# Optimization experiments

Hardware: AMD Instinct MI355X
Metric: run time of the kernel (lower is better)

## Reference

```python
import jax, jax.numpy as jnp
import numpy as np

WS = (8, 8)          # window size
NUM_HEADS = 16
C = 512
B_ = 2048            # batch * num_windows
NW = 256             # num_windows per image (mask dim)
N = WS[0] * WS[1]    # tokens per window = 64


def _relative_position_index():
    coords = np.stack(np.meshgrid(np.arange(WS[0]), np.arange(WS[1]), indexing='ij'))  # [2,Wh,Ww]
    flat = coords.reshape(2, -1)                         # [2,N]
    rel = flat[:, :, None] - flat[:, None, :]            # [2,N,N]
    rel = rel.transpose(1, 2, 0).astype(np.int32)        # [N,N,2]
    rel[..., 0] += WS[0] - 1
    rel[..., 1] += WS[1] - 1
    rel[..., 0] *= 2 * WS[1] - 1
    return jnp.asarray(rel.sum(-1))                      # [N,N] in [0, 225)


def setup_inputs() -> dict:
    key = jax.random.key(0)
    ks = jax.random.split(key, 8)
    return {
        'x': jax.random.normal(ks[0], (B_, N, C), jnp.float32),
        'mask': jax.random.normal(ks[1], (NW, N, N), jnp.float32),
        'qkv_w': jax.random.normal(ks[2], (3 * C, C), jnp.float32) * 0.02,
        'q_bias': jax.random.normal(ks[3], (C,), jnp.float32) * 0.02,
        'v_bias': jax.random.normal(ks[4], (C,), jnp.float32) * 0.02,
        'rpb_table': jax.random.normal(ks[5], ((2 * WS[0] - 1) * (2 * WS[1] - 1), NUM_HEADS), jnp.float32) * 0.02,
        'proj_w': jax.random.normal(ks[6], (C, C), jnp.float32) * 0.02,
        'proj_b': jax.random.normal(ks[7], (C,), jnp.float32) * 0.02,
        'rel_index': _relative_position_index(),
    }


def reference(x, mask, qkv_w, q_bias, v_bias, rpb_table, proj_w, proj_b, rel_index):
    Bw, n, c = x.shape
    h = NUM_HEADS
    d = c // h
    # qkv with bias = [q_bias, 0, v_bias]
    qkv_b = jnp.concatenate([q_bias, jnp.zeros_like(v_bias), v_bias])
    qkv = x @ qkv_w.T + qkv_b                               # [B_,N,3C]
    qkv = qkv.reshape(Bw, n, 3, h, d).transpose(2, 0, 3, 1, 4)
    q, k, v = qkv[0], qkv[1], qkv[2]                        # each [B_,h,N,d]
    scale = d ** -0.5
    attn = jnp.einsum('bhnd,bhmd->bhnm', q * scale, k)      # [B_,h,N,N]
    # gathered relative position bias
    rpb = rpb_table[rel_index.reshape(-1)].reshape(n, n, h).transpose(2, 0, 1)  # [h,N,N]
    attn = attn + rpb[None]
    nW = mask.shape[0]
    attn = attn.reshape(Bw // nW, nW, h, n, n) + mask[None, :, None]
    attn = jax.nn.softmax(attn.reshape(Bw, h, n, n), axis=-1)
    out = jnp.einsum('bhnm,bhmd->bhnd', attn, v)            # [B_,h,N,d]
    out = out.transpose(0, 2, 1, 3).reshape(Bw, n, c)
    return out @ proj_w.T + proj_b
```

## Files before the change

kernel.cpp:

```cpp
#include <hip/hip_runtime.h>

typedef short s16x8 __attribute__((ext_vector_type(8)));
typedef float f32x4 __attribute__((ext_vector_type(4)));

__device__ __forceinline__ unsigned short f2bf(float f) {
    unsigned int u = __builtin_bit_cast(unsigned int, f);
    u += 0x7fffu + ((u >> 16) & 1u);
    return (unsigned short)(u >> 16);
}

__device__ __forceinline__ void gload16(const void* g, void* l) {
    __builtin_amdgcn_global_load_lds(
        (const __attribute__((address_space(1))) unsigned int*)g,
        (__attribute__((address_space(3))) unsigned int*)l,
        16, 0, 0);
}

__global__ void cast_bf16_kernel(const float* __restrict__ src,
                                 unsigned short* __restrict__ dst, int n4) {
    int i = blockIdx.x * 256 + threadIdx.x;
    if (i >= n4) return;
    float4 v = ((const float4*)src)[i];
    ushort4 o;
    o.x = f2bf(v.x); o.y = f2bf(v.y); o.z = f2bf(v.z); o.w = f2bf(v.w);
    ((ushort4*)dst)[i] = o;
}

__global__ void rpb_kernel(const float* __restrict__ table,
                           const int* __restrict__ rel,
                           float* __restrict__ rpb) {
    int t = blockIdx.x * 64 + threadIdx.x;
    int idx = rel[t];
#pragma unroll
    for (int h = 0; h < 16; ++h)
        rpb[h * 4096 + t] = table[idx * 16 + h];
}

template <bool SW>
__device__ __forceinline__ void kloop128(const unsigned short* __restrict__ Ab,
                                         const unsigned short* __restrict__ Bb,
                                         unsigned short* Al, unsigned short* Bl,
                                         int t, int wave, int ln, int hk,
                                         int wr, int wc, f32x4 (&acc)[4][4]) {
    const int row = t >> 2, cg = t & 3;
    for (int k0 = 0; k0 < 512; k0 += 32) {
        gload16(Ab + (size_t)row * 512 + k0 + cg * 8, &Al[wave * 512]);
        gload16(Ab + (size_t)(row + 64) * 512 + k0 + cg * 8, &Al[2048 + wave * 512]);
        gload16(Bb + (size_t)row * 512 + k0 + cg * 8, &Bl[wave * 512]);
        gload16(Bb + (size_t)(row + 64) * 512 + k0 + cg * 8, &Bl[2048 + wave * 512]);
        __syncthreads();
        s16x8 af[4], bf[4];
#pragma unroll
        for (int i = 0; i < 4; ++i)
            af[i] = *(const s16x8*)&Al[(wr + i * 16 + ln) * 32 + hk * 8];
#pragma unroll
        for (int j = 0; j < 4; ++j)
            bf[j] = *(const s16x8*)&Bl[(wc + j * 16 + ln) * 32 + hk * 8];
#pragma unroll
        for (int i = 0; i < 4; ++i)
#pragma unroll
            for (int j = 0; j < 4; ++j) {
                if constexpr (SW)
                    acc[j][i] = __builtin_amdgcn_mfma_f32_16x16x32_bf16(bf[j], af[i], acc[j][i], 0, 0, 0);
                else
                    acc[i][j] = __builtin_amdgcn_mfma_f32_16x16x32_bf16(af[i], bf[j], acc[i][j], 0, 0, 0);
            }
        __syncthreads();
    }
}

template <int MODE, int NCOLS>
__global__ __launch_bounds__(256) void gemm_bt(
    const unsigned short* __restrict__ A, const unsigned short* __restrict__ B,
    const float* __restrict__ bq, const float* __restrict__ bv,
    unsigned short* __restrict__ qb, unsigned short* __restrict__ kb,
    unsigned short* __restrict__ vtb,
    const float* __restrict__ pb, float* __restrict__ out) {
    __shared__ unsigned short smem[8192];
    unsigned short* Al = smem;
    unsigned short* Bl = smem + 4096;

    constexpr int NBN = NCOLS / 128;
    const unsigned int cpx = gridDim.x >> 3;
    const unsigned int wg = (blockIdx.x & 7u) * cpx + (blockIdx.x >> 3);
    const int bm = wg / NBN;
    const int bn = wg % NBN;
    const int t = threadIdx.x;
    const int wave = t >> 6, lane = t & 63;
    const int ln = lane & 15, hk = lane >> 4;
    const int wr = (wave >> 1) * 64, wc = (wave & 1) * 64;

    const f32x4 zero = {0.f, 0.f, 0.f, 0.f};
    f32x4 acc[4][4];
#pragma unroll
    for (int i = 0; i < 4; ++i)
#pragma unroll
        for (int j = 0; j < 4; ++j) acc[i][j] = zero;

    const unsigned short* Ab = A + (size_t)bm * 128 * 512;
    const unsigned short* Bb = B + (size_t)bn * 128 * 512;

    if constexpr (MODE == 1) {
        kloop128<true>(Ab, Bb, Al, Bl, t, wave, ln, hk, wr, wc, acc);
#pragma unroll
        for (int j = 0; j < 4; ++j) {
            const int nn0 = bn * 128 + wc + j * 16 + hk * 4;
            const float4 b4 = *(const float4*)&pb[nn0];
#pragma unroll
            for (int i = 0; i < 4; ++i) {
                const int m = bm * 128 + wr + i * 16 + ln;
                float4 o4;
                o4.x = acc[j][i][0] + b4.x;
                o4.y = acc[j][i][1] + b4.y;
                o4.z = acc[j][i][2] + b4.z;
                o4.w = acc[j][i][3] + b4.w;
                *(float4*)(out + (size_t)m * NCOLS + nn0) = o4;
            }
        }
    } else {
        const int which = bn >> 2;
        const int bb = bm * 2;
        if (which < 2) {
            kloop128<true>(Ab, Bb, Al, Bl, t, wave, ln, hk, wr, wc, acc);
            unsigned short* dst0 = (which == 0) ? qb : kb;
#pragma unroll
            for (int j = 0; j < 4; ++j) {
                const int colT0 = wc + j * 16 + hk * 4;
                const int rem0 = (bn * 128 + colT0) & 511;
                float4 b4 = {0.f, 0.f, 0.f, 0.f};
                if (which == 0) b4 = *(const float4*)&bq[rem0];
                const int head = rem0 >> 5;
                const int dd0 = rem0 & 31;
#pragma unroll
                for (int i = 0; i < 4; ++i) {
                    const int tokL = wr + i * 16 + ln;
                    const size_t bh = (size_t)((bb + (tokL >> 6)) * 16 + head);
                    ushort4 pk;
                    pk.x = f2bf(acc[j][i][0] + b4.x);
                    pk.y = f2bf(acc[j][i][1] + b4.y);
                    pk.z = f2bf(acc[j][i][2] + b4.z);
                    pk.w = f2bf(acc[j][i][3] + b4.w);
                    *(ushort4*)(dst0 + bh * 2048 + (size_t)(tokL & 63) * 32 + dd0) = pk;
                }
            }
        } else {
            kloop128<false>(Ab, Bb, Al, Bl, t, wave, ln, hk, wr, wc, acc);
#pragma unroll
            for (int i = 0; i < 4; ++i) {
                const int tok0L = wr + i * 16 + hk * 4;
                const size_t bhbase = (size_t)(bb + (tok0L >> 6)) * 16;
                const int tok0 = tok0L & 63;
#pragma unroll
                for (int j = 0; j < 4; ++j) {
                    const int rem = (bn * 128 + wc + j * 16 + ln) & 511;
                    const float bias = bv[rem];
                    const int head = rem >> 5, dd = rem & 31;
                    ushort4 pk;
                    pk.x = f2bf(acc[i][j][0] + bias);
                    pk.y = f2bf(acc[i][j][1] + bias);
                    pk.z = f2bf(acc[i][j][2] + bias);
                    pk.w = f2bf(acc[i][j][3] + bias);
                    *(ushort4*)(vtb + (bhbase + head) * 2048 + (size_t)dd * 64 + tok0) = pk;
                }
            }
        }
    }
}

__global__ __launch_bounds__(256) void attn_kernel(
    const unsigned short* __restrict__ qbuf, const unsigned short* __restrict__ kbuf,
    const unsigned short* __restrict__ vtbuf, const float* __restrict__ rpb,
    const float* __restrict__ mask, unsigned short* __restrict__ aout) {
    __shared__ unsigned short ql[64 * 32];
    __shared__ unsigned short kl[64 * 32];
    __shared__ unsigned short vl[32 * 64];
    __shared__ unsigned short plds[64 * 64];

    const int bh = blockIdx.x;
    const int b = bh >> 4, head = bh & 15;
    const int wmask = b & 255;
    const int t = threadIdx.x, wave = t >> 6, lane = t & 63;
    const int ln = lane & 15, hk = lane >> 4;

    const size_t base = (size_t)bh * 2048;
    gload16(qbuf + base + t * 8, &ql[wave * 512]);
    gload16(kbuf + base + t * 8, &kl[wave * 512]);
    gload16(vtbuf + base + t * 8, &vl[wave * 512]);
    __syncthreads();

    const f32x4 zero = {0.f, 0.f, 0.f, 0.f};
    s16x8 aq = *(const s16x8*)&ql[(wave * 16 + ln) * 32 + hk * 8];
    f32x4 sc[4];
#pragma unroll
    for (int j = 0; j < 4; ++j) {
        s16x8 bk = *(const s16x8*)&kl[(j * 16 + ln) * 32 + hk * 8];
        sc[j] = __builtin_amdgcn_mfma_f32_16x16x32_bf16(aq, bk, zero, 0, 0, 0);
    }

    const float scale = 0.17677669529663687f;
    const float* rpb_h = rpb + head * 4096;
    const float* msk = mask + wmask * 4096;

    float p[4][4];
#pragma unroll
    for (int r = 0; r < 4; ++r) {
        const int i = wave * 16 + hk * 4 + r;
        float v[4], m = -1e30f;
#pragma unroll
        for (int j = 0; j < 4; ++j) {
            const int c = j * 16 + ln;
            v[j] = sc[j][r] * scale + rpb_h[i * 64 + c] + msk[i * 64 + c];
            m = fmaxf(m, v[j]);
        }
        for (int off = 1; off < 16; off <<= 1) m = fmaxf(m, __shfl_xor(m, off));
        float s = 0.f;
#pragma unroll
        for (int j = 0; j < 4; ++j) { v[j] = __expf(v[j] - m); s += v[j]; }
        for (int off = 1; off < 16; off <<= 1) s += __shfl_xor(s, off);
        const float inv = 1.f / s;
#pragma unroll
        for (int j = 0; j < 4; ++j) p[r][j] = v[j] * inv;
    }
#pragma unroll
    for (int r = 0; r < 4; ++r)
#pragma unroll
        for (int j = 0; j < 4; ++j)
            plds[(wave * 16 + hk * 4 + r) * 64 + j * 16 + ln] = f2bf(p[r][j]);
    __syncthreads();

    f32x4 o2[2] = {zero, zero};
#pragma unroll
    for (int kt = 0; kt < 2; ++kt) {
        s16x8 ap = *(const s16x8*)&plds[(wave * 16 + ln) * 64 + kt * 32 + hk * 8];
#pragma unroll
        for (int nt = 0; nt < 2; ++nt) {
            s16x8 bvf = *(const s16x8*)&vl[(nt * 16 + ln) * 64 + kt * 32 + hk * 8];
            o2[nt] = __builtin_amdgcn_mfma_f32_16x16x32_bf16(bvf, ap, o2[nt], 0, 0, 0);
        }
    }
#pragma unroll
    for (int nt = 0; nt < 2; ++nt) {
        ushort4 pk;
        pk.x = f2bf(o2[nt][0]); pk.y = f2bf(o2[nt][1]);
        pk.z = f2bf(o2[nt][2]); pk.w = f2bf(o2[nt][3]);
        *(ushort4*)(aout + ((size_t)(b * 64 + wave * 16 + ln)) * 512
                    + head * 32 + nt * 16 + hk * 4) = pk;
    }
}

extern "C" void kernel_launch(void* const* d_in, const int* in_sizes, int n_in,
                              void* d_out, int out_size, void* d_ws, size_t ws_size,
                              hipStream_t stream) {
    const float* x      = (const float*)d_in[0];
    const float* mask   = (const float*)d_in[1];
    const float* qkv_w  = (const float*)d_in[2];
    const float* q_bias = (const float*)d_in[3];
    const float* v_bias = (const float*)d_in[4];
    const float* rpb_t  = (const float*)d_in[5];
    const float* proj_w = (const float*)d_in[6];
    const float* proj_b = (const float*)d_in[7];
    const int*   rel    = (const int*)d_in[8];
    float* out = (float*)d_out;

    char* ws = (char*)d_ws;
    unsigned short* xbf   = (unsigned short*)ws;
    unsigned short* qbuf  = (unsigned short*)(ws + 0x08000000);
    unsigned short* kbuf  = (unsigned short*)(ws + 0x10000000);
    unsigned short* vtbuf = (unsigned short*)(ws + 0x18000000);
    unsigned short* wqkv  = (unsigned short*)(ws + 0x20000000);
    unsigned short* wproj = (unsigned short*)(ws + 0x20180000);
    float*          rpb   = (float*)(ws + 0x20200000);
    unsigned short* aout  = xbf;

    cast_bf16_kernel<<<65536, 256, 0, stream>>>(x, xbf, 16777216);
    cast_bf16_kernel<<<768, 256, 0, stream>>>(qkv_w, wqkv, 196608);
    cast_bf16_kernel<<<256, 256, 0, stream>>>(proj_w, wproj, 65536);
    rpb_kernel<<<64, 64, 0, stream>>>(rpb_t, rel, rpb);

    gemm_bt<0, 1536><<<1024 * 12, 256, 0, stream>>>(
        xbf, wqkv, q_bias, v_bias, qbuf, kbuf, vtbuf, nullptr, nullptr);

    attn_kernel<<<32768, 256, 0, stream>>>(qbuf, kbuf, vtbuf, rpb, mask, aout);

    gemm_bt<1, 512><<<1024 * 4, 256, 0, stream>>>(
        aout, wproj, nullptr, nullptr, nullptr, nullptr, nullptr, proj_b, out);
}
```

Measured before the change: 1.137 ms.

## Stage GEMM and attention epilogues through LDS for coalesced 16-byte stores

The GEMM epilogues for the output projection and for Q, K and V^T are rewritten to stage each wave's tile in padded shared memory, then write contiguous rows with wide vector stores instead of scattered 8-byte ones. The attention kernel's output is staged the same way. It also removes the barrier before the P·V step, since each wave reads back only its own P rows, and pads the P rows to reduce bank conflicts. The cost is extra LDS traffic and a larger GEMM shared buffer, which may lower occupancy.

```diff
diff --git a/kernel.cpp b/kernel.cpp
--- a/kernel.cpp
+++ b/kernel.cpp
@@ -76,7 +76,7 @@
     unsigned short* __restrict__ qb, unsigned short* __restrict__ kb,
     unsigned short* __restrict__ vtb,
     const float* __restrict__ pb, float* __restrict__ out) {
-    __shared__ unsigned short smem[8192];
+    __shared__ __align__(16) unsigned short smem[10240];
     unsigned short* Al = smem;
     unsigned short* Bl = smem + 4096;
 
@@ -102,65 +102,97 @@
 
     if constexpr (MODE == 1) {
         kloop128<true>(Ab, Bb, Al, Bl, t, wave, ln, hk, wr, wc, acc);
+        float* epf = (float*)smem + wave * 1280;
 #pragma unroll
         for (int j = 0; j < 4; ++j) {
             const int nn0 = bn * 128 + wc + j * 16 + hk * 4;
             const float4 b4 = *(const float4*)&pb[nn0];
 #pragma unroll
             for (int i = 0; i < 4; ++i) {
-                const int m = bm * 128 + wr + i * 16 + ln;
+                const int tk = i * 16 + ln;
                 float4 o4;
                 o4.x = acc[j][i][0] + b4.x;
                 o4.y = acc[j][i][1] + b4.y;
                 o4.z = acc[j][i][2] + b4.z;
                 o4.w = acc[j][i][3] + b4.w;
-                *(float4*)(out + (size_t)m * NCOLS + nn0) = o4;
+                *(float4*)&epf[tk * 20 + hk * 4] = o4;
+            }
+            const int nnb = bn * 128 + wc + j * 16;
+#pragma unroll
+            for (int rr = 0; rr < 4; ++rr) {
+                const int li = rr * 64 + lane;
+                const int tk = li >> 2, c4 = (li & 3) * 4;
+                float4 v4 = *(const float4*)&epf[tk * 20 + c4];
+                *(float4*)(out + (size_t)(bm * 128 + wr + tk) * NCOLS + nnb + c4) = v4;
             }
         }
     } else {
         const int which = bn >> 2;
         const int bb = bm * 2;
+        const size_t winbase = (size_t)((bb + (wr >> 6)) * 16);
+        unsigned short* ep = smem + wave * 2560;
         if (which < 2) {
             kloop128<true>(Ab, Bb, Al, Bl, t, wave, ln, hk, wr, wc, acc);
             unsigned short* dst0 = (which == 0) ? qb : kb;
 #pragma unroll
-            for (int j = 0; j < 4; ++j) {
-                const int colT0 = wc + j * 16 + hk * 4;
-                const int rem0 = (bn * 128 + colT0) & 511;
-                float4 b4 = {0.f, 0.f, 0.f, 0.f};
-                if (which == 0) b4 = *(const float4*)&bq[rem0];
-                const int head = rem0 >> 5;
-                const int dd0 = rem0 & 31;
-#pragma unroll
-                for (int i = 0; i < 4; ++i) {
-                    const int tokL = wr + i * 16 + ln;
-                    const size_t bh = (size_t)((bb + (tokL >> 6)) * 16 + head);
-                    ushort4 pk;
-                    pk.x = f2bf(acc[j][i][0] + b4.x);
-                    pk.y = f2bf(acc[j][i][1] + b4.y);
-                    pk.z = f2bf(acc[j][i][2] + b4.z);
-                    pk.w = f2bf(acc[j][i][3] + b4.w);
-                    *(ushort4*)(dst0 + bh * 2048 + (size_t)(tokL & 63) * 32 + dd0) = pk;
+            for (int H = 0; H < 2; ++H) {
+#pragma unroll
+                for (int j2 = 0; j2 < 2; ++j2) {
+                    const int j = H * 2 + j2;
+                    const int rem0 = (bn * 128 + wc + j * 16 + hk * 4) & 511;
+                    float4 b4 = {0.f, 0.f, 0.f, 0.f};
+                    if (which == 0) b4 = *(const float4*)&bq[rem0];
+                    const int ch0 = j2 * 16 + hk * 4;
+#pragma unroll
+                    for (int i = 0; i < 4; ++i) {
+                        const int tk = i * 16 + ln;
+                        ushort4 pk;
+                        pk.x = f2bf(acc[j][i][0] + b4.x);
+                        pk.y = f2bf(acc[j][i][1] + b4.y);
+                        pk.z = f2bf(acc[j][i][2] + b4.z);
+                        pk.w = f2bf(acc[j][i][3] + b4.w);
+                        *(ushort4*)&ep[tk * 40 + ch0] = pk;
+                    }
+                }
+                const int remH = (bn * 128 + wc + H * 32) & 511;
+                const size_t Dq = (winbase + (remH >> 5)) * 2048;
+#pragma unroll
+                for (int rr = 0; rr < 4; ++rr) {
+                    const int li = rr * 64 + lane;
+                    const int tk = li >> 2, c8 = (li & 3) * 8;
+                    s16x8 val = *(const s16x8*)&ep[tk * 40 + c8];
+                    *(s16x8*)(dst0 + Dq + tk * 32 + c8) = val;
                 }
             }
         } else {
             kloop128<false>(Ab, Bb, Al, Bl, t, wave, ln, hk, wr, wc, acc);
 #pragma unroll
-            for (int i = 0; i < 4; ++i) {
-                const int tok0L = wr + i * 16 + hk * 4;
-                const size_t bhbase = (size_t)(bb + (tok0L >> 6)) * 16;
-                const int tok0 = tok0L & 63;
-#pragma unroll
-                for (int j = 0; j < 4; ++j) {
+            for (int H = 0; H < 2; ++H) {
+#pragma unroll
+                for (int j2 = 0; j2 < 2; ++j2) {
+                    const int j = H * 2 + j2;
                     const int rem = (bn * 128 + wc + j * 16 + ln) & 511;
                     const float bias = bv[rem];
-                    const int head = rem >> 5, dd = rem & 31;
-                    ushort4 pk;
-                    pk.x = f2bf(acc[i][j][0] + bias);
-                    pk.y = f2bf(acc[i][j][1] + bias);
-                    pk.z = f2bf(acc[i][j][2] + bias);
-                    pk.w = f2bf(acc[i][j][3] + bias);
-                    *(ushort4*)(vtb + (bhbase + head) * 2048 + (size_t)dd * 64 + tok0) = pk;
+                    const int ch = j2 * 16 + ln;
+#pragma unroll
+                    for (int i = 0; i < 4; ++i) {
+                        const int tk = i * 16 + hk * 4;
+                        ushort4 pk;
+                        pk.x = f2bf(acc[i][j][0] + bias);
+                        pk.y = f2bf(acc[i][j][1] + bias);
+                        pk.z = f2bf(acc[i][j][2] + bias);
+                        pk.w = f2bf(acc[i][j][3] + bias);
+                        *(ushort4*)&ep[ch * 72 + tk] = pk;
+                    }
+                }
+                const int remH = (bn * 128 + wc + H * 32) & 511;
+                const size_t Dv = (winbase + (remH >> 5)) * 2048;
+#pragma unroll
+                for (int rr = 0; rr < 4; ++rr) {
+                    const int li = rr * 64 + lane;
+                    const int dd = li >> 3, t8 = (li & 7) * 8;
+                    s16x8 val = *(const s16x8*)&ep[dd * 72 + t8];
+                    *(s16x8*)(vtb + Dv + dd * 64 + t8) = val;
                 }
             }
         }
@@ -171,10 +203,10 @@
     const unsigned short* __restrict__ qbuf, const unsigned short* __restrict__ kbuf,
     const unsigned short* __restrict__ vtbuf, const float* __restrict__ rpb,
     const float* __restrict__ mask, unsigned short* __restrict__ aout) {
-    __shared__ unsigned short ql[64 * 32];
-    __shared__ unsigned short kl[64 * 32];
-    __shared__ unsigned short vl[32 * 64];
-    __shared__ unsigned short plds[64 * 64];
+    __shared__ __align__(16) unsigned short ql[64 * 32];
+    __shared__ __align__(16) unsigned short kl[64 * 32];
+    __shared__ __align__(16) unsigned short vl[32 * 64];
+    __shared__ __align__(16) unsigned short plds[64 * 72];
 
     const int bh = blockIdx.x;
     const int b = bh >> 4, head = bh & 15;
@@ -225,27 +257,29 @@
     for (int r = 0; r < 4; ++r)
 #pragma unroll
         for (int j = 0; j < 4; ++j)
-            plds[(wave * 16 + hk * 4 + r) * 64 + j * 16 + ln] = f2bf(p[r][j]);
-    __syncthreads();
+            plds[(wave * 16 + hk * 4 + r) * 72 + j * 16 + ln] = f2bf(p[r][j]);
 
     f32x4 o2[2] = {zero, zero};
 #pragma unroll
     for (int kt = 0; kt < 2; ++kt) {
-        s16x8 ap = *(const s16x8*)&plds[(wave * 16 + ln) * 64 + kt * 32 + hk * 8];
+        s16x8 ap = *(const s16x8*)&plds[(wave * 16 + ln) * 72 + kt * 32 + hk * 8];
 #pragma unroll
         for (int nt = 0; nt < 2; ++nt) {
             s16x8 bvf = *(const s16x8*)&vl[(nt * 16 + ln) * 64 + kt * 32 + hk * 8];
             o2[nt] = __builtin_amdgcn_mfma_f32_16x16x32_bf16(bvf, ap, o2[nt], 0, 0, 0);
         }
     }
+    unsigned short* ep = plds + wave * 1152;
 #pragma unroll
     for (int nt = 0; nt < 2; ++nt) {
         ushort4 pk;
         pk.x = f2bf(o2[nt][0]); pk.y = f2bf(o2[nt][1]);
         pk.z = f2bf(o2[nt][2]); pk.w = f2bf(o2[nt][3]);
-        *(ushort4*)(aout + ((size_t)(b * 64 + wave * 16 + ln)) * 512
-                    + head * 32 + nt * 16 + hk * 4) = pk;
-    }
+        *(ushort4*)&ep[ln * 40 + nt * 16 + hk * 4] = pk;
+    }
+    const int tk = lane >> 2, c8 = (lane & 3) * 8;
+    s16x8 val = *(const s16x8*)&ep[tk * 40 + c8];
+    *(s16x8*)(aout + ((size_t)(b * 64 + wave * 16 + tk)) * 512 + head * 32 + c8) = val;
 }
 
 extern "C" void kernel_launch(void* const* d_in, const int* in_sizes, int n_in,
```

Result: faster. 1.061 ms (-6.7%).
